# Performance work log

Measured on AMD Instinct MI355X. Metric: run time of the kernel, lower is better.

## Reference

```python
import jax, jax.numpy as jnp
import numpy as np

N = 50000        # nodes
E = 800000       # edges (avg degree 16)
D_IN = 19        # in_channels(16) + 2 coords + 1 observed flag
H = 64           # graph_hidden
L = 3            # graph_layers
EPS = 1e-5       # BatchNorm eps


def setup_inputs() -> dict:
    key = jax.random.key(0)
    ks = jax.random.split(key, 12)
    s = 0.05
    x = jax.random.normal(ks[0], (N, D_IN), jnp.float32)
    edge_index = jax.random.randint(ks[1], (2, E), 0, N, dtype=jnp.int32)
    return {
        "x": x,
        "edge_index": edge_index,
        # input projection + input BN
        "w_in": jax.random.normal(ks[2], (D_IN, H), jnp.float32) * s,
        "b_in": jnp.zeros((H,), jnp.float32),
        "bn0_g": jnp.ones((H,), jnp.float32),
        "bn0_b": jnp.zeros((H,), jnp.float32),
        # per-layer SAGEConv: lin_l (aggregated neighbors, with bias), lin_r (self, no bias)
        "wl": jax.random.normal(ks[3], (L, H, H), jnp.float32) * s,
        "bl": jnp.zeros((L, H), jnp.float32),
        "wr": jax.random.normal(ks[4], (L, H, H), jnp.float32) * s,
        # per-layer BatchNorm affine
        "bn_g": jnp.ones((L, H), jnp.float32),
        "bn_b": jnp.zeros((L, H), jnp.float32),
    }


def _batchnorm(h, g, b):
    # training-mode BN over the node axis (biased variance, like torch)
    mu = h.mean(axis=0)
    var = h.var(axis=0)
    return (h - mu) * jax.lax.rsqrt(var + EPS) * g + b


def reference(x, edge_index, w_in, b_in, bn0_g, bn0_b, wl, bl, wr, bn_g, bn_b):
    src = edge_index[0]
    dst = edge_index[1]
    n = x.shape[0]

    # input_proj -> BN -> ReLU  (dropout is identity at inference)
    h = x @ w_in + b_in
    h = jax.nn.relu(_batchnorm(h, bn0_g, bn0_b))

    # in-degree for mean aggregation (computed once)
    deg = jax.ops.segment_sum(jnp.ones((src.shape[0],), h.dtype), dst, num_segments=n)
    denom = jnp.maximum(deg, 1.0)[:, None]

    for l in range(L):
        # SAGEConv(mean): gather source feats, segment-mean into targets
        msgs = h[src]                                        # [E, H] gather
        agg = jax.ops.segment_sum(msgs, dst, num_segments=n) / denom
        h_new = agg @ wl[l] + bl[l] + h @ wr[l]
        h_new = jax.nn.relu(_batchnorm(h_new, bn_g[l], bn_b[l]))
        h = h + h_new                                        # residual
    return h
```

## Files before the change

kernel.cpp:

```cpp
#include <hip/hip_runtime.h>
#include <hip/hip_bf16.h>

#define NODES 50000
#define EDGES 800000
#define DIN   19
#define LAYERS 3
#define BN_EPS 1e-5f

#define NBINS 196
#define EPB   4096
#define NBLK  196
#define NTILES 782
#define G0TILES 196
#define TPB   256

typedef __attribute__((ext_vector_type(4))) float f32x4;
typedef __attribute__((ext_vector_type(2))) float f32x2;
typedef __attribute__((ext_vector_type(8))) short s16x8;

__device__ inline ushort bf16bits(float f) {
    __hip_bfloat16 h = __float2bfloat16(f);
    return *reinterpret_cast<ushort*>(&h);
}
__device__ inline float bf16val(ushort u) { return __uint_as_float((unsigned)u << 16); }

#if __has_builtin(__builtin_amdgcn_cvt_pk_f32_fp8) && __has_builtin(__builtin_amdgcn_cvt_pk_fp8_f32)
__device__ inline unsigned pack4_fp8(float a, float b, float c, float d) {
    unsigned w = __builtin_amdgcn_cvt_pk_fp8_f32(a, b, 0u, false);
    return __builtin_amdgcn_cvt_pk_fp8_f32(c, d, w, true);
}
__device__ inline void acc4_fp8(unsigned v, float* a) {
    f32x2 lo = __builtin_amdgcn_cvt_pk_f32_fp8(v, false);
    f32x2 hi = __builtin_amdgcn_cvt_pk_f32_fp8(v, true);
    a[0] += lo.x; a[1] += lo.y; a[2] += hi.x; a[3] += hi.y;
}
#else
__device__ inline unsigned enc1(float f) {
    _Float16 hf = (_Float16)f;
    unsigned u = (unsigned)*reinterpret_cast<unsigned short*>(&hf);
    u = (u + 0x7Fu + ((u >> 8) & 1u)) >> 8;
    return u & 0xFFu;
}
__device__ inline float dec1(unsigned b) {
    unsigned short u = (unsigned short)(b << 8);
    _Float16 hf = *reinterpret_cast<_Float16*>(&u);
    return (float)hf;
}
__device__ inline unsigned pack4_fp8(float a, float b, float c, float d) {
    return enc1(a) | (enc1(b) << 8) | (enc1(c) << 16) | (enc1(d) << 24);
}
__device__ inline void acc4_fp8(unsigned v, float* a) {
    a[0] += dec1(v & 0xFF); a[1] += dec1((v >> 8) & 0xFF);
    a[2] += dec1((v >> 16) & 0xFF); a[3] += dec1(v >> 24);
}
#endif


__global__ void k_prep(const float* __restrict__ w_in, const float* __restrict__ wl,
                       const float* __restrict__ wr, ushort* __restrict__ WiT,
                       ushort* __restrict__ WcatT, int* __restrict__ bintot,
                       float* __restrict__ stats) {
    int i0 = blockIdx.x * blockDim.x + threadIdx.x;
    int stride = gridDim.x * blockDim.x;
    for (int i = i0; i < NBINS; i += stride) bintot[i] = 0;
    for (int i = i0; i < 4 * 2048; i += stride) stats[i] = 0.0f;
    for (int i = i0; i < 64 * 32; i += stride) {
        int c = i >> 5, k = i & 31;
        WiT[i] = bf16bits(k < DIN ? w_in[k * 64 + c] : 0.0f);
    }
    for (int i = i0; i < LAYERS * 64 * 128; i += stride) {
        int l = i >> 13, rem = i & 8191;
        int c = rem >> 7, k = rem & 127;
        float v = (k < 64) ? wl[(l * 64 + k) * 64 + c] : wr[(l * 64 + (k - 64)) * 64 + c];
        WcatT[i] = bf16bits(v);
    }
}


union SMemK2 {
    struct { int hist[256], cur[256], wsum[4]; unsigned stage[EPB]; } sort;
    struct { ushort xt[256][40]; float red[4][4][128]; } g0;
};

__device__ inline void do_sortA(int blk, int t, const int* __restrict__ src,
                                const int* __restrict__ dst, int2* __restrict__ cb,
                                int* __restrict__ bintot, unsigned* __restrict__ bbuf,
                                SMemK2& sm) {
    int e0 = blk * EPB;
    int ne = min(EPB, EDGES - e0);
    int d[4]; unsigned pk[4];
    #pragma unroll
    for (int i = 0; i < 4; ++i) {
        int j = t + i * 1024;
        if (j < ne) {
            int dd = dst[e0 + j];
            d[i] = dd;
            pk[i] = ((unsigned)(dd & 255) << 24) | (unsigned)src[e0 + j];
        } else d[i] = -1;
    }
    if (t < 256) sm.sort.hist[t] = 0;
    __syncthreads();
    #pragma unroll
    for (int i = 0; i < 4; ++i)
        if (d[i] >= 0) atomicAdd(&sm.sort.hist[d[i] >> 8], 1);
    __syncthreads();
    int ln = t & 63, wv = t >> 6;
    int cntv = 0, inc = 0;
    if (t < 256) {
        cntv = sm.sort.hist[t];
        inc = cntv;
        #pragma unroll
        for (int s = 1; s < 64; s <<= 1) {
            int u = __shfl_up(inc, s);
            if (ln >= s) inc += u;
        }
        if (ln == 63) sm.sort.wsum[wv] = inc;
    }
    __syncthreads();
    if (t < 256) {
        int woff = 0;
        #pragma unroll
        for (int i = 0; i < 4; ++i) if (i < wv) woff += sm.sort.wsum[i];
        int excl = woff + inc - cntv;
        sm.sort.cur[t] = excl;
        if (t < NBINS) {
            cb[t * NBLK + blk] = make_int2(excl, cntv);
            if (cntv) atomicAdd(&bintot[t], cntv);
        }
    }
    __syncthreads();
    #pragma unroll
    for (int i = 0; i < 4; ++i)
        if (d[i] >= 0) {
            int slot = atomicAdd(&sm.sort.cur[d[i] >> 8], 1);
            sm.sort.stage[slot] = pk[i];
        }
    __syncthreads();
    #pragma unroll
    for (int i = 0; i < 4; ++i) {
        int j = t + i * 1024;
        if (j < ne) bbuf[e0 + j] = sm.sort.stage[j];
    }
}

__device__ inline void do_gemm0(int tile, int t, const float* __restrict__ x,
                                const ushort* __restrict__ WiT, const float* __restrict__ bias,
                                ushort* __restrict__ tb, float* __restrict__ stats,
                                SMemK2& sm) {
    int base = tile * 256;
    int nv = min(256, NODES - base);
    unsigned* xz = (unsigned*)sm.g0.xt;
    for (int i = t; i < 256 * 20; i += 1024) xz[i] = 0;
    __syncthreads();
    const float* xs = x + (size_t)base * DIN;
    for (int e = t; e < nv * DIN; e += 1024) {
        int n = e / DIN, k = e - n * DIN;
        sm.g0.xt[n][k] = bf16bits(xs[e]);
    }
    __syncthreads();
    int grp = t >> 8, tl = t & 255;
    int lane = t & 63, wl = (tl >> 6);
    int r = lane & 15, g = lane >> 4;
    f32x4 acc[4] = {{0.f,0.f,0.f,0.f},{0.f,0.f,0.f,0.f},{0.f,0.f,0.f,0.f},{0.f,0.f,0.f,0.f}};
    s16x8 af = *(const s16x8*)&sm.g0.xt[grp * 64 + wl * 16 + r][g * 8];
    #pragma unroll
    for (int j = 0; j < 4; ++j) {
        s16x8 bf = *(const s16x8*)(WiT + (size_t)(j * 16 + r) * 32 + g * 8);
        acc[j] = __builtin_amdgcn_mfma_f32_16x16x32_bf16(af, bf, acc[j], 0, 0, 0);
    }
    int row0 = base + grp * 64 + wl * 16;
    float s_[4], q_[4];
    #pragma unroll
    for (int j = 0; j < 4; ++j) {
        float b = bias[j * 16 + r];
        float s = 0.0f, q = 0.0f;
        #pragma unroll
        for (int i = 0; i < 4; ++i) {
            int row = row0 + g * 4 + i;
            if (row < NODES) {
                float v = acc[j][i] + b;
                tb[(size_t)row * 64 + j * 16 + r] = bf16bits(v);
                s += v; q += v * v;
            }
        }
        s += __shfl_xor(s, 16); s += __shfl_xor(s, 32);
        q += __shfl_xor(q, 16); q += __shfl_xor(q, 32);
        s_[j] = s; q_[j] = q;
    }
    if (g == 0) {
        #pragma unroll
        for (int j = 0; j < 4; ++j) {
            sm.g0.red[grp][wl][j * 16 + r] = s_[j];
            sm.g0.red[grp][wl][64 + j * 16 + r] = q_[j];
        }
    }
    __syncthreads();
    if (tl < 128) {
        float tot = sm.g0.red[grp][0][tl] + sm.g0.red[grp][1][tl] +
                    sm.g0.red[grp][2][tl] + sm.g0.red[grp][3][tl];
        atomicAdd(&stats[tl * 16], tot);
    }
}

__global__ __launch_bounds__(1024) void k_sort_g0(const int* __restrict__ esrc, const int* __restrict__ edst,
                                                  int2* __restrict__ cb, int* __restrict__ bintot,
                                                  unsigned* __restrict__ bbuf,
                                                  const float* __restrict__ x, const ushort* __restrict__ WiT,
                                                  const float* __restrict__ bias, ushort* __restrict__ tb,
                                                  float* __restrict__ stats) {
    __shared__ SMemK2 sm;
    int t = threadIdx.x;
    if (blockIdx.x < NBLK) do_sortA(blockIdx.x, t, esrc, edst, cb, bintot, bbuf, sm);
    else                   do_gemm0(blockIdx.x - NBLK, t, x, WiT, bias, tb, stats, sm);
}


struct SMemApplyR {
    ushort hn[64][72];
};

__device__ inline void do_applyR(int rb, int t, int l,
                                 const ushort* __restrict__ tb, const float* __restrict__ stats,
                                 const float* __restrict__ gamma, const float* __restrict__ beta,
                                 float* __restrict__ h, unsigned* __restrict__ hb8,
                                 const ushort* __restrict__ WcatT, const float* __restrict__ bl,
                                 ushort* __restrict__ tb2, int residual, SMemApplyR& sm) {
    const float invN = 1.0f / NODES;
    int base = rb * 64;
    int nv = min(64, NODES - base);
    for (int idx = t; idx < nv * 16; idx += TPB) {
        int n = base + (idx >> 4);
        int j = (idx & 15) * 4;
        ushort4 tv = *(const ushort4*)(tb + (size_t)n * 64 + j);
        float tf[4] = { bf16val(tv.x), bf16val(tv.y), bf16val(tv.z), bf16val(tv.w) };
        f32x4 hv;
        if (residual) hv = *(const f32x4*)(h + (size_t)n * 64 + j);
        float out[4];
        #pragma unroll
        for (int k = 0; k < 4; ++k) {
            int f = j + k;
            float mu = stats[f * 16] * invN;
            float var = stats[(64 + f) * 16] * invN - mu * mu;
            float sc = gamma[f] * rsqrtf(var + BN_EPS);
            float sh = beta[f] - mu * sc;
            float v = fmaxf(tf[k] * sc + sh, 0.0f);
            out[k] = residual ? (hv[k] + v) : v;
            sm.hn[idx >> 4][j + k] = bf16bits(out[k]);
        }
        *(f32x4*)(h + (size_t)n * 64 + j) = f32x4{out[0], out[1], out[2], out[3]};
        hb8[(size_t)n * 16 + (idx & 15)] = pack4_fp8(out[0], out[1], out[2], out[3]);
    }
    __syncthreads();
    int lane = t & 63, wave = t >> 6;
    int r = lane & 15, g = lane >> 4;
    f32x4 acc[4] = {{0.f,0.f,0.f,0.f},{0.f,0.f,0.f,0.f},{0.f,0.f,0.f,0.f},{0.f,0.f,0.f,0.f}};
    #pragma unroll
    for (int k0 = 0; k0 < 64; k0 += 32) {
        s16x8 af = *(const s16x8*)&sm.hn[wave * 16 + r][k0 + g * 8];
        #pragma unroll
        for (int j = 0; j < 4; ++j) {
            s16x8 bf = *(const s16x8*)(WcatT + (size_t)l * 8192 + (size_t)(j * 16 + r) * 128 + 64 + k0 + g * 8);
            acc[j] = __builtin_amdgcn_mfma_f32_16x16x32_bf16(af, bf, acc[j], 0, 0, 0);
        }
    }
    #pragma unroll
    for (int j = 0; j < 4; ++j) {
        float b = bl[j * 16 + r];
        #pragma unroll
        for (int i = 0; i < 4; ++i) {
            int row = base + wave * 16 + g * 4 + i;
            if (row < NODES) tb2[(size_t)row * 64 + j * 16 + r] = bf16bits(acc[j][i] + b);
        }
    }
}

__global__ __launch_bounds__(TPB) void k_applyR(const ushort* __restrict__ tb, const float* __restrict__ stats,
                                                const float* __restrict__ gamma, const float* __restrict__ beta,
                                                float* __restrict__ h, unsigned* __restrict__ hb8,
                                                const ushort* __restrict__ WcatT, const float* __restrict__ bl,
                                                ushort* __restrict__ tb2, int l, int residual) {
    __shared__ SMemApplyR sm;
    do_applyR(blockIdx.x, threadIdx.x, l, tb, stats, gamma, beta, h, hb8, WcatT, bl, tb2, residual, sm);
}


__device__ inline int ubound(const int* pre, int f) {
    int lo = 0, hi = NBLK;
    while (lo + 1 < hi) {
        int mid = (lo + hi) >> 1;
        if (pre[mid] <= f) lo = mid; else hi = mid;
    }
    return lo;
}

struct SMemBinB {
    int red[256];
    int segoff[NBLK], segcnt[NBLK], pre[NBLK + 1];
    int deg[256], loff[256], cur[256];
    int wsum4[4];
};

union SMemK3 {
    SMemBinB binb;
    SMemApplyR ar;
};

__device__ inline void do_binB(int b, int t, const int2* __restrict__ cb,
                               const int* __restrict__ bintot, const unsigned* __restrict__ bbuf,
                               int* __restrict__ off, float* __restrict__ rden,
                               int* __restrict__ ebuf, SMemBinB& sm) {
    int ln = t & 63, wv = t >> 6;
    sm.red[t] = (t < b) ? bintot[t] : 0;
    __syncthreads();
    #pragma unroll
    for (int s = 128; s > 0; s >>= 1) {
        if (t < s) sm.red[t] += sm.red[t + s];
        __syncthreads();
    }
    int binoff = sm.red[0];
    if (t < NBLK) {
        int2 c = cb[b * NBLK + t];
        sm.segoff[t] = c.x; sm.segcnt[t] = c.y;
    }
    sm.deg[t] = 0; sm.cur[t] = 0;
    __syncthreads();
    if (wv == 0) {
        int carry = 0;
        for (int base = 0; base < NBLK; base += 64) {
            int idx = base + ln;
            int v = (idx < NBLK) ? sm.segcnt[idx] : 0;
            int inc = v;
            #pragma unroll
            for (int s = 1; s < 64; s <<= 1) {
                int u = __shfl_up(inc, s);
                if (ln >= s) inc += u;
            }
            if (idx < NBLK) sm.pre[idx] = carry + inc - v;
            carry += __shfl(inc, 63);
        }
        if (ln == 0) sm.pre[NBLK] = carry;
    }
    __syncthreads();
    int total = sm.pre[NBLK];
    for (int f = t; f < total; f += TPB) {
        int sg = ubound(sm.pre, f);
        unsigned e = bbuf[sg * EPB + sm.segoff[sg] + (f - sm.pre[sg])];
        atomicAdd(&sm.deg[e >> 24], 1);
    }
    __syncthreads();
    int dv = sm.deg[t], inc2 = dv;
    #pragma unroll
    for (int s = 1; s < 64; s <<= 1) {
        int u = __shfl_up(inc2, s);
        if (ln >= s) inc2 += u;
    }
    if (ln == 63) sm.wsum4[wv] = inc2;
    __syncthreads();
    int woff = 0;
    #pragma unroll
    for (int i = 0; i < 4; ++i) if (i < wv) woff += sm.wsum4[i];
    int excl = woff + inc2 - dv;
    sm.loff[t] = excl;
    int node = (b << 8) + t;
    if (node < NODES) {
        off[node] = binoff + excl;
        rden[node] = 1.0f / fmaxf((float)dv, 1.0f);
    }
    if (b == NBINS - 1 && t == 0) off[NODES] = EDGES;
    __syncthreads();
    for (int f = t; f < total; f += TPB) {
        int sg = ubound(sm.pre, f);
        unsigned e = bbuf[sg * EPB + sm.segoff[sg] + (f - sm.pre[sg])];
        int dd = e >> 24;
        int slot = atomicAdd(&sm.cur[dd], 1);
        ebuf[binoff + sm.loff[dd] + slot] = (int)(e & 0xFFFFFFu);
    }
}

__global__ __launch_bounds__(TPB) void k_csr_ar0(const int2* __restrict__ cb, const int* __restrict__ bintot,
                                                 const unsigned* __restrict__ bbuf,
                                                 int* __restrict__ off, float* __restrict__ rden,
                                                 int* __restrict__ ebuf,
                                                 const ushort* __restrict__ tb, const float* __restrict__ stats,
                                                 const float* __restrict__ gamma, const float* __restrict__ beta,
                                                 float* __restrict__ h, unsigned* __restrict__ hb8,
                                                 const ushort* __restrict__ WcatT, const float* __restrict__ bl,
                                                 ushort* __restrict__ tb2) {
    __shared__ SMemK3 sm;
    int t = threadIdx.x;
    if (blockIdx.x < NBINS)
        do_binB(blockIdx.x, t, cb, bintot, bbuf, off, rden, ebuf, sm.binb);
    else
        do_applyR(blockIdx.x - NBINS, t, 0, tb, stats, gamma, beta, h, hb8, WcatT, bl, tb2, 0, sm.ar);
}


__global__ __launch_bounds__(TPB) void k_gemmL(const ushort* __restrict__ AB, const ushort* __restrict__ WcatT,
                                               const ushort* __restrict__ tb2, ushort* __restrict__ tb,
                                               float* __restrict__ stats, int l) {
    __shared__ float red[4][128];
    int t = threadIdx.x;
    int lane = t & 63, wave = t >> 6;
    int row0 = blockIdx.x * 64;
    int r = lane & 15, g = lane >> 4;
    f32x4 acc[4] = {{0.f,0.f,0.f,0.f},{0.f,0.f,0.f,0.f},{0.f,0.f,0.f,0.f},{0.f,0.f,0.f,0.f}};
    int ar = row0 + wave * 16 + r;
    if (ar >= NODES) ar = NODES - 1;
    #pragma unroll
    for (int k0 = 0; k0 < 64; k0 += 32) {
        s16x8 af = *(const s16x8*)(AB + (size_t)ar * 64 + k0 + g * 8);
        #pragma unroll
        for (int j = 0; j < 4; ++j) {
            s16x8 bf = *(const s16x8*)(WcatT + (size_t)l * 8192 + (size_t)(j * 16 + r) * 128 + k0 + g * 8);
            acc[j] = __builtin_amdgcn_mfma_f32_16x16x32_bf16(af, bf, acc[j], 0, 0, 0);
        }
    }
    float s_[4], q_[4];
    #pragma unroll
    for (int j = 0; j < 4; ++j) {
        float s = 0.0f, q = 0.0f;
        #pragma unroll
        for (int i = 0; i < 4; ++i) {
            int row = row0 + wave * 16 + g * 4 + i;
            if (row < NODES) {
                float v = acc[j][i] + bf16val(tb2[(size_t)row * 64 + j * 16 + r]);
                tb[(size_t)row * 64 + j * 16 + r] = bf16bits(v);
                s += v; q += v * v;
            }
        }
        s += __shfl_xor(s, 16); s += __shfl_xor(s, 32);
        q += __shfl_xor(q, 16); q += __shfl_xor(q, 32);
        s_[j] = s; q_[j] = q;
    }
    if (g == 0) {
        #pragma unroll
        for (int j = 0; j < 4; ++j) {
            red[wave][j * 16 + r] = s_[j];
            red[wave][64 + j * 16 + r] = q_[j];
        }
    }
    __syncthreads();
    if (t < 128) {
        float tot = red[0][t] + red[1][t] + red[2][t] + red[3][t];
        atomicAdd(&stats[t * 16], tot);
    }
}


__global__ void k_apply_fin(const ushort* __restrict__ tb, const float* __restrict__ stats,
                            const float* __restrict__ gamma, const float* __restrict__ beta,
                            float* __restrict__ h) {
    int idx0 = blockIdx.x * blockDim.x + threadIdx.x;
    int stride = gridDim.x * blockDim.x;
    const float invN = 1.0f / NODES;
    for (int idx = idx0; idx < NODES * 16; idx += stride) {
        int n = idx >> 4;
        int j = (idx & 15) * 4;
        ushort4 tv = *(const ushort4*)(tb + (size_t)n * 64 + j);
        float tf[4] = { bf16val(tv.x), bf16val(tv.y), bf16val(tv.z), bf16val(tv.w) };
        f32x4 hv = *(const f32x4*)(h + (size_t)n * 64 + j);
        float out[4];
        #pragma unroll
        for (int k = 0; k < 4; ++k) {
            int f = j + k;
            float mu = stats[f * 16] * invN;
            float var = stats[(64 + f) * 16] * invN - mu * mu;
            float sc = gamma[f] * rsqrtf(var + BN_EPS);
            float sh = beta[f] - mu * sc;
            out[k] = hv[k] + fmaxf(tf[k] * sc + sh, 0.0f);
        }
        *(f32x4*)(h + (size_t)n * 64 + j) = f32x4{out[0], out[1], out[2], out[3]};
    }
}


__global__ void k_agg(const int* __restrict__ off, const int* __restrict__ ebuf,
                      const float* __restrict__ rden, const unsigned* __restrict__ hb8,
                      ushort* __restrict__ ABh) {
    const uint2* H2 = (const uint2*)hb8;
    uint4* AB4 = (uint4*)ABh;
    int t = threadIdx.x;
    int lane = t & 63;
    int q = lane >> 3;
    int fl = lane & 7;
    int w = blockIdx.x * (blockDim.x >> 6) + (t >> 6);
    int nw = gridDim.x * (blockDim.x >> 6);
    for (int n = w; n < NODES; n += nw) {
        int p0 = off[n], p1 = off[n + 1];
        float a[8] = {0.f,0.f,0.f,0.f,0.f,0.f,0.f,0.f};
        int p = p0 + q;
        for (; p + 8 < p1; p += 16) {
            int s0 = ebuf[p], s1 = ebuf[p + 8];
            uint2 v0 = H2[(size_t)s0 * 8 + fl];
            uint2 v1 = H2[(size_t)s1 * 8 + fl];
            acc4_fp8(v0.x, a); acc4_fp8(v0.y, a + 4);
            acc4_fp8(v1.x, a); acc4_fp8(v1.y, a + 4);
        }
        for (; p < p1; p += 8) {
            uint2 v = H2[(size_t)ebuf[p] * 8 + fl];
            acc4_fp8(v.x, a); acc4_fp8(v.y, a + 4);
        }
        #pragma unroll
        for (int i = 0; i < 8; ++i) {
            a[i] += __shfl_xor(a[i], 8);
            a[i] += __shfl_xor(a[i], 16);
            a[i] += __shfl_xor(a[i], 32);
        }
        if (q == 0) {
            float rd = rden[n];
            uint4 o;
            o.x = (unsigned)bf16bits(a[0] * rd) | ((unsigned)bf16bits(a[1] * rd) << 16);
            o.y = (unsigned)bf16bits(a[2] * rd) | ((unsigned)bf16bits(a[3] * rd) << 16);
            o.z = (unsigned)bf16bits(a[4] * rd) | ((unsigned)bf16bits(a[5] * rd) << 16);
            o.w = (unsigned)bf16bits(a[6] * rd) | ((unsigned)bf16bits(a[7] * rd) << 16);
            AB4[(size_t)n * 8 + fl] = o;
        }
    }
}


extern "C" void kernel_launch(void* const* d_in, const int* in_sizes, int n_in,
                              void* d_out, int out_size, void* d_ws, size_t ws_size,
                              hipStream_t stream) {
    const float* x    = (const float*)d_in[0];
    const int*   ei   = (const int*)d_in[1];
    const float* w_in = (const float*)d_in[2];
    const float* b_in = (const float*)d_in[3];
    const float* bn0g = (const float*)d_in[4];
    const float* bn0b = (const float*)d_in[5];
    const float* wl   = (const float*)d_in[6];
    const float* bl   = (const float*)d_in[7];
    const float* wr   = (const float*)d_in[8];
    const float* bng  = (const float*)d_in[9];
    const float* bnb  = (const float*)d_in[10];
    const int* esrc = ei;
    const int* edst = ei + EDGES;
    float* h = (float*)d_out;

    char* p = (char*)d_ws;
    auto alloc = [&](size_t bytes) {
        char* r = p;
        p += (bytes + 255) & ~size_t(255);
        return r;
    };
    int*      bintot = (int*)alloc((size_t)NBINS * 4);
    float*    stats  = (float*)alloc((size_t)4 * 2048 * 4);
    int2*     cb     = (int2*)alloc((size_t)NBINS * NBLK * 8);
    unsigned* bbuf   = (unsigned*)alloc((size_t)NBLK * EPB * 4);
    int*      off    = (int*)alloc((size_t)(NODES + 1) * 4);
    float*    rden   = (float*)alloc((size_t)NODES * 4);
    int*      ebuf   = (int*)alloc((size_t)EDGES * 4);
    ushort*   WiT    = (ushort*)alloc(64 * 32 * 2);
    ushort*   WcatT  = (ushort*)alloc(LAYERS * 64 * 128 * 2);
    ushort*   tb     = (ushort*)alloc((size_t)NODES * 64 * 2);
    ushort*   tb2    = (ushort*)alloc((size_t)NODES * 64 * 2);
    ushort*   AB     = (ushort*)alloc((size_t)NODES * 64 * 2);
    unsigned* hb8    = (unsigned*)alloc((size_t)NODES * 16 * 4);

    k_prep<<<128, TPB, 0, stream>>>(w_in, wl, wr, WiT, WcatT, bintot, stats);
    k_sort_g0<<<NBLK + G0TILES, 1024, 0, stream>>>(esrc, edst, cb, bintot, bbuf,
                                                   x, WiT, b_in, tb, stats);
    k_csr_ar0<<<NBINS + NTILES, TPB, 0, stream>>>(cb, bintot, bbuf, off, rden, ebuf,
                                                  tb, stats, bn0g, bn0b, h, hb8,
                                                  WcatT, bl + 0 * 64, tb2);

    for (int l = 0; l < LAYERS; ++l) {
        k_agg<<<2048, TPB, 0, stream>>>(off, ebuf, rden, hb8, AB);
        k_gemmL<<<NTILES, TPB, 0, stream>>>(AB, WcatT, tb2, tb, stats + (l + 1) * 2048, l);
        if (l < LAYERS - 1) {
            k_applyR<<<NTILES, TPB, 0, stream>>>(tb, stats + (l + 1) * 2048, bng + l * 64,
                                                 bnb + l * 64, h, hb8, WcatT,
                                                 bl + (l + 1) * 64, tb2, l + 1, 1);
        } else {
            k_apply_fin<<<2048, TPB, 0, stream>>>(tb, stats + (l + 1) * 2048, bng + l * 64,
                                                  bnb + l * 64, h);
        }
    }
}
```

Measured before the change: 261.3 us.

## Fuse neighbor aggregation into the per-layer GEMM via shared-memory tile

Merges the separate aggregation kernel and the lin_l GEMM kernel into one kernel. Each 512-thread block aggregates 32 nodes into an LDS tile, then runs the MFMA GEMM on that tile and accumulates the BN statistics. This removes the global round trip of the aggregated bf16 matrix and one launch per layer. In exchange, blocks are smaller (32 rows), there are more atomic stat updates, and the block must wait at a barrier for its slowest gather before any GEMM work starts.

```diff
diff --git a/kernel.cpp b/kernel.cpp
--- a/kernel.cpp
+++ b/kernel.cpp
@@ -11,6 +11,7 @@
 #define EPB   4096
 #define NBLK  196
 #define NTILES 782
+#define AGT   1563
 #define G0TILES 196
 #define TPB   256
 
@@ -395,54 +396,81 @@
 }
 
 
-__global__ __launch_bounds__(TPB) void k_gemmL(const ushort* __restrict__ AB, const ushort* __restrict__ WcatT,
-                                               const ushort* __restrict__ tb2, ushort* __restrict__ tb,
-                                               float* __restrict__ stats, int l) {
-    __shared__ float red[4][128];
+__global__ __launch_bounds__(512, 8) void k_aggemm(const int* __restrict__ off, const int* __restrict__ ebuf,
+                                                   const float* __restrict__ rden, const unsigned* __restrict__ hb8,
+                                                   const ushort* __restrict__ WcatT, const ushort* __restrict__ tb2,
+                                                   ushort* __restrict__ tb, float* __restrict__ stats, int l) {
+    __shared__ ushort aggt[32][72];
+    __shared__ float red[8][2][16];
     int t = threadIdx.x;
-    int lane = t & 63, wave = t >> 6;
-    int row0 = blockIdx.x * 64;
+    int wv = t >> 6, lane = t & 63;
+    int q = lane >> 3, fl = lane & 7;
+    int base = blockIdx.x * 32;
+    const uint2* H2 = (const uint2*)hb8;
+    #pragma unroll 1
+    for (int i = 0; i < 4; ++i) {
+        int row = wv * 4 + i;
+        int n = base + row;
+        float a[8] = {0.f,0.f,0.f,0.f,0.f,0.f,0.f,0.f};
+        if (n < NODES) {
+            int p0 = off[n], p1 = off[n + 1];
+            int p = p0 + q;
+            for (; p + 8 < p1; p += 16) {
+                int s0 = ebuf[p], s1 = ebuf[p + 8];
+                uint2 v0 = H2[(size_t)s0 * 8 + fl];
+                uint2 v1 = H2[(size_t)s1 * 8 + fl];
+                acc4_fp8(v0.x, a); acc4_fp8(v0.y, a + 4);
+                acc4_fp8(v1.x, a); acc4_fp8(v1.y, a + 4);
+            }
+            for (; p < p1; p += 8) {
+                uint2 v = H2[(size_t)ebuf[p] * 8 + fl];
+                acc4_fp8(v.x, a); acc4_fp8(v.y, a + 4);
+            }
+        }
+        #pragma unroll
+        for (int k = 0; k < 8; ++k) {
+            a[k] += __shfl_xor(a[k], 8);
+            a[k] += __shfl_xor(a[k], 16);
+            a[k] += __shfl_xor(a[k], 32);
+        }
+        if (q == 0) {
+            float rd = (n < NODES) ? rden[n] : 0.0f;
+            uint4 o;
+            o.x = (unsigned)bf16bits(a[0] * rd) | ((unsigned)bf16bits(a[1] * rd) << 16);
+            o.y = (unsigned)bf16bits(a[2] * rd) | ((unsigned)bf16bits(a[3] * rd) << 16);
+            o.z = (unsigned)bf16bits(a[4] * rd) | ((unsigned)bf16bits(a[5] * rd) << 16);
+            o.w = (unsigned)bf16bits(a[6] * rd) | ((unsigned)bf16bits(a[7] * rd) << 16);
+            *(uint4*)&aggt[row][fl * 8] = o;
+        }
+    }
+    __syncthreads();
+    int rowq = wv >> 2, colq = wv & 3;
     int r = lane & 15, g = lane >> 4;
-    f32x4 acc[4] = {{0.f,0.f,0.f,0.f},{0.f,0.f,0.f,0.f},{0.f,0.f,0.f,0.f},{0.f,0.f,0.f,0.f}};
-    int ar = row0 + wave * 16 + r;
-    if (ar >= NODES) ar = NODES - 1;
+    f32x4 acc = {0.f, 0.f, 0.f, 0.f};
     #pragma unroll
     for (int k0 = 0; k0 < 64; k0 += 32) {
-        s16x8 af = *(const s16x8*)(AB + (size_t)ar * 64 + k0 + g * 8);
-        #pragma unroll
-        for (int j = 0; j < 4; ++j) {
-            s16x8 bf = *(const s16x8*)(WcatT + (size_t)l * 8192 + (size_t)(j * 16 + r) * 128 + k0 + g * 8);
-            acc[j] = __builtin_amdgcn_mfma_f32_16x16x32_bf16(af, bf, acc[j], 0, 0, 0);
-        }
-    }
-    float s_[4], q_[4];
-    #pragma unroll
-    for (int j = 0; j < 4; ++j) {
-        float s = 0.0f, q = 0.0f;
-        #pragma unroll
-        for (int i = 0; i < 4; ++i) {
-            int row = row0 + wave * 16 + g * 4 + i;
-            if (row < NODES) {
-                float v = acc[j][i] + bf16val(tb2[(size_t)row * 64 + j * 16 + r]);
-                tb[(size_t)row * 64 + j * 16 + r] = bf16bits(v);
-                s += v; q += v * v;
-            }
-        }
-        s += __shfl_xor(s, 16); s += __shfl_xor(s, 32);
-        q += __shfl_xor(q, 16); q += __shfl_xor(q, 32);
-        s_[j] = s; q_[j] = q;
-    }
-    if (g == 0) {
-        #pragma unroll
-        for (int j = 0; j < 4; ++j) {
-            red[wave][j * 16 + r] = s_[j];
-            red[wave][64 + j * 16 + r] = q_[j];
-        }
-    }
+        s16x8 af = *(const s16x8*)&aggt[rowq * 16 + r][k0 + g * 8];
+        s16x8 bf = *(const s16x8*)(WcatT + (size_t)l * 8192 + (size_t)(colq * 16 + r) * 128 + k0 + g * 8);
+        acc = __builtin_amdgcn_mfma_f32_16x16x32_bf16(af, bf, acc, 0, 0, 0);
+    }
+    float s = 0.0f, qq = 0.0f;
+    #pragma unroll
+    for (int i = 0; i < 4; ++i) {
+        int row = base + rowq * 16 + g * 4 + i;
+        if (row < NODES) {
+            float v = acc[i] + bf16val(tb2[(size_t)row * 64 + colq * 16 + r]);
+            tb[(size_t)row * 64 + colq * 16 + r] = bf16bits(v);
+            s += v; qq += v * v;
+        }
+    }
+    s += __shfl_xor(s, 16); s += __shfl_xor(s, 32);
+    qq += __shfl_xor(qq, 16); qq += __shfl_xor(qq, 32);
+    if (g == 0) { red[wv][0][r] = s; red[wv][1][r] = qq; }
     __syncthreads();
     if (t < 128) {
-        float tot = red[0][t] + red[1][t] + red[2][t] + red[3][t];
-        atomicAdd(&stats[t * 16], tot);
+        int f = t & 63, st = t >> 6;
+        float val = red[f >> 4][st][f & 15] + red[4 + (f >> 4)][st][f & 15];
+        atomicAdd(&stats[(st * 64 + f) * 16], val);
     }
 }
 
@@ -470,51 +498,6 @@
             out[k] = hv[k] + fmaxf(tf[k] * sc + sh, 0.0f);
         }
         *(f32x4*)(h + (size_t)n * 64 + j) = f32x4{out[0], out[1], out[2], out[3]};
-    }
-}
-
-
-__global__ void k_agg(const int* __restrict__ off, const int* __restrict__ ebuf,
-                      const float* __restrict__ rden, const unsigned* __restrict__ hb8,
-                      ushort* __restrict__ ABh) {
-    const uint2* H2 = (const uint2*)hb8;
-    uint4* AB4 = (uint4*)ABh;
-    int t = threadIdx.x;
-    int lane = t & 63;
-    int q = lane >> 3;
-    int fl = lane & 7;
-    int w = blockIdx.x * (blockDim.x >> 6) + (t >> 6);
-    int nw = gridDim.x * (blockDim.x >> 6);
-    for (int n = w; n < NODES; n += nw) {
-        int p0 = off[n], p1 = off[n + 1];
-        float a[8] = {0.f,0.f,0.f,0.f,0.f,0.f,0.f,0.f};
-        int p = p0 + q;
-        for (; p + 8 < p1; p += 16) {
-            int s0 = ebuf[p], s1 = ebuf[p + 8];
-            uint2 v0 = H2[(size_t)s0 * 8 + fl];
-            uint2 v1 = H2[(size_t)s1 * 8 + fl];
-            acc4_fp8(v0.x, a); acc4_fp8(v0.y, a + 4);
-            acc4_fp8(v1.x, a); acc4_fp8(v1.y, a + 4);
-        }
-        for (; p < p1; p += 8) {
-            uint2 v = H2[(size_t)ebuf[p] * 8 + fl];
-            acc4_fp8(v.x, a); acc4_fp8(v.y, a + 4);
-        }
-        #pragma unroll
-        for (int i = 0; i < 8; ++i) {
-            a[i] += __shfl_xor(a[i], 8);
-            a[i] += __shfl_xor(a[i], 16);
-            a[i] += __shfl_xor(a[i], 32);
-        }
-        if (q == 0) {
-            float rd = rden[n];
-            uint4 o;
-            o.x = (unsigned)bf16bits(a[0] * rd) | ((unsigned)bf16bits(a[1] * rd) << 16);
-            o.y = (unsigned)bf16bits(a[2] * rd) | ((unsigned)bf16bits(a[3] * rd) << 16);
-            o.z = (unsigned)bf16bits(a[4] * rd) | ((unsigned)bf16bits(a[5] * rd) << 16);
-            o.w = (unsigned)bf16bits(a[6] * rd) | ((unsigned)bf16bits(a[7] * rd) << 16);
-            AB4[(size_t)n * 8 + fl] = o;
-        }
     }
 }
 
@@ -554,7 +537,6 @@
     ushort*   WcatT  = (ushort*)alloc(LAYERS * 64 * 128 * 2);
     ushort*   tb     = (ushort*)alloc((size_t)NODES * 64 * 2);
     ushort*   tb2    = (ushort*)alloc((size_t)NODES * 64 * 2);
-    ushort*   AB     = (ushort*)alloc((size_t)NODES * 64 * 2);
     unsigned* hb8    = (unsigned*)alloc((size_t)NODES * 16 * 4);
 
     k_prep<<<128, TPB, 0, stream>>>(w_in, wl, wr, WiT, WcatT, bintot, stats);
@@ -565,8 +547,8 @@
                                                   WcatT, bl + 0 * 64, tb2);
 
     for (int l = 0; l < LAYERS; ++l) {
-        k_agg<<<2048, TPB, 0, stream>>>(off, ebuf, rden, hb8, AB);
-        k_gemmL<<<NTILES, TPB, 0, stream>>>(AB, WcatT, tb2, tb, stats + (l + 1) * 2048, l);
+        k_aggemm<<<AGT, 512, 0, stream>>>(off, ebuf, rden, hb8, WcatT, tb2, tb,
+                                          stats + (l + 1) * 2048, l);
         if (l < LAYERS - 1) {
             k_applyR<<<NTILES, TPB, 0, stream>>>(tb, stats + (l + 1) * 2048, bng + l * 64,
                                                  bnb + l * 64, h, hb8, WcatT,
```

Result: slower. 281.4 us (+7.7%).
